# Kernel tuning notes

Measured on AMD Instinct MI355X. Metric: run time of the kernel, lower is better.

Reference implementation:

```python
import jax, jax.numpy as jnp
import numpy as np

D_MODEL, D_K, D_V, N_HEADS, D_FF = 1024, 64, 64, 16, 2736
EPS_NORM = 1e-12   # F.normalize eps
EPS_RMS = 1e-6     # RMSNorm eps


def _rmsnorm(x, g):
    return x * jax.lax.rsqrt(jnp.mean(x * x, axis=-1, keepdims=True) + EPS_RMS) * g


def _l2norm(x):
    n = jnp.sqrt(jnp.sum(x * x, axis=-1, keepdims=True))
    return x / jnp.maximum(n, EPS_NORM)


def setup_inputs() -> dict:
    key = jax.random.key(0)
    ks = jax.random.split(key, 10)
    B, T = 2, 1024
    s_in = 0.1 / np.sqrt(D_MODEL)   # xavier-like small init, gain 0.1
    s_ff = 0.1 / np.sqrt(D_FF)
    return {
        "x": jax.random.normal(ks[0], (B, T, D_MODEL), jnp.float32),
        "Wq": jax.random.normal(ks[1], (D_MODEL, N_HEADS * D_K), jnp.float32) * s_in,
        "Wk": jax.random.normal(ks[2], (D_MODEL, N_HEADS * D_K), jnp.float32) * s_in,
        "Wv": jax.random.normal(ks[3], (D_MODEL, N_HEADS * D_V), jnp.float32) * s_in,
        "Wg": jax.random.normal(ks[4], (D_MODEL, N_HEADS * D_K), jnp.float32) * s_in,
        "Wo": jax.random.normal(ks[5], (N_HEADS * D_V, D_MODEL), jnp.float32) * s_in,
        "w1": jax.random.normal(ks[6], (D_MODEL, D_FF), jnp.float32) * s_in,
        "w2": jax.random.normal(ks[7], (D_MODEL, D_FF), jnp.float32) * s_in,
        "w3": jax.random.normal(ks[8], (D_FF, D_MODEL), jnp.float32) * s_ff,
        "g_attn": jnp.ones((D_MODEL,), jnp.float32),
        "g_ffn": jnp.ones((D_MODEL,), jnp.float32),
    }


def _gla(h, Wq, Wk, Wv, Wg, Wo):
    B, T, _ = h.shape
    q = _l2norm((h @ Wq).reshape(B, T, N_HEADS, D_K))
    k = _l2norm((h @ Wk).reshape(B, T, N_HEADS, D_K))
    v = (h @ Wv).reshape(B, T, N_HEADS, D_V)
    alpha = jax.nn.sigmoid(h @ Wg).reshape(B, T, N_HEADS, D_K)

    def step(S, inp):
        a_t, k_t, v_t, q_t = inp                       # [B,H,dk],[B,H,dk],[B,H,dv],[B,H,dk]
        S = a_t[..., None] * S + k_t[..., None] * v_t[..., None, :]   # [B,H,dk,dv]
        o_t = jnp.einsum('bhkv,bhk->bhv', S, q_t)
        return S, o_t

    S0 = jnp.zeros((B, N_HEADS, D_K, D_V), h.dtype)
    xs = (jnp.swapaxes(alpha, 0, 1), jnp.swapaxes(k, 0, 1),
          jnp.swapaxes(v, 0, 1), jnp.swapaxes(q, 0, 1))  # time-major [T,B,H,*]
    _, o = jax.lax.scan(step, S0, xs)                    # o: [T,B,H,dv]
    o = jnp.swapaxes(o, 0, 1).reshape(B, T, N_HEADS * D_V)
    return o @ Wo


def reference(x, Wq, Wk, Wv, Wg, Wo, w1, w2, w3, g_attn, g_ffn):
    # Pre-LN GLA block: x -> Norm -> GLA -> +res -> Norm -> SwiGLU -> +res
    h = _rmsnorm(x, g_attn)
    x = x + _gla(h, Wq, Wk, Wv, Wg, Wo)
    h = _rmsnorm(x, g_ffn)
    ffn = (jax.nn.silu(h @ w1) * (h @ w2)) @ w3
    return x + ffn
```

## Files before the change

kernel.cpp:

```cpp
#include <hip/hip_runtime.h>

typedef unsigned short ushort_t;
typedef unsigned int uint32;
typedef short short8 __attribute__((ext_vector_type(8)));
typedef unsigned short ushort4v __attribute__((ext_vector_type(4)));
typedef float f32x4 __attribute__((ext_vector_type(4)));

#define MROWS 2048
#define DMODEL 1024
#define NH 16
#define DFF 2736
#define DFFP 2752
#define NBH 32

__device__ __forceinline__ float b2f(ushort_t u) {
  return __builtin_bit_cast(float, ((uint32)u) << 16);
}
__device__ __forceinline__ ushort_t f2b(float f) {
  uint32 u = __builtin_bit_cast(uint32, f);
  return (ushort_t)((u + 0x7FFFu + ((u >> 16) & 1u)) >> 16);
}
__device__ __forceinline__ float san(float v) {
  uint32 u = __builtin_bit_cast(uint32, v);
  return (((u >> 23) & 0xFFu) == 0xFFu) ? 0.0f : v;
}
__device__ __forceinline__ float sclamp(float v, float lim) {
  return fminf(fmaxf(san(v), -lim), lim);
}

typedef const __attribute__((address_space(1))) unsigned int* gas_ptr;
typedef __attribute__((address_space(3))) unsigned int* las_ptr;
__device__ __forceinline__ void gl_lds16(const void* g, void* l) {
  __builtin_amdgcn_global_load_lds((gas_ptr)g, (las_ptr)l, 16, 0, 0);
}

__device__ __forceinline__ void rmsnorm_body(
    const float* __restrict__ x, const float* __restrict__ g,
    ushort_t* __restrict__ out, int row, int tid) {
  size_t base = (size_t)row * DMODEL;
  int c0 = tid * 4;
  float4 t = *(const float4*)(x + base + c0);
  float v[4] = {t.x, t.y, t.z, t.w};
  float s = v[0]*v[0] + v[1]*v[1] + v[2]*v[2] + v[3]*v[3];
  for (int off = 32; off > 0; off >>= 1) s += __shfl_xor(s, off);
  __shared__ float red[4];
  int wave = tid >> 6, lane = tid & 63;
  if (lane == 0) red[wave] = s;
  __syncthreads();
  if (tid == 0) {
    float tt = red[0] + red[1] + red[2] + red[3];
    red[0] = rsqrtf(tt * (1.0f / DMODEL) + 1e-6f);
  }
  __syncthreads();
  float sc = red[0];
  float4 gg = *(const float4*)(g + c0);
  float gv[4] = {gg.x, gg.y, gg.z, gg.w};
  for (int j = 0; j < 4; ++j)
    out[base + c0 + j] = f2b(sclamp(v[j] * sc * gv[j], 1e4f));
}

__global__ __launch_bounds__(256) void rmsnorm_kernel(
    const float* __restrict__ x, const float* __restrict__ g,
    ushort_t* __restrict__ out) {
  rmsnorm_body(x, g, out, blockIdx.x, threadIdx.x);
}

__device__ __forceinline__ void transpose_tile(
    const float* __restrict__ src, ushort_t* __restrict__ d,
    int K, int N, int Kpad, int n0, int k0, int tid) {
  __shared__ ushort_t tile[32][33];
  int tx = tid & 31, ty = tid >> 5;
  #pragma unroll
  for (int i = 0; i < 4; ++i) {
    int k = k0 + ty + i * 8, n = n0 + tx;
    float v = (k < K && n < N) ? src[(size_t)k * N + n] : 0.0f;
    tile[ty + i * 8][tx] = f2b(v);
  }
  __syncthreads();
  #pragma unroll
  for (int i = 0; i < 4; ++i) {
    int r = ty + i * 8;
    d[(size_t)(n0 + r) * Kpad + k0 + tx] = tile[tx][r];
  }
}

__global__ __launch_bounds__(256) void transpose_kernel(
    const float* __restrict__ S0, const float* __restrict__ S1,
    const float* __restrict__ S2, const float* __restrict__ S3,
    ushort_t* __restrict__ dst, int K, int N, int Kpad, int Npad) {
  const float* src = (blockIdx.z == 0) ? S0 : (blockIdx.z == 1) ? S1
                   : (blockIdx.z == 2) ? S2 : S3;
  ushort_t* d = dst + (size_t)blockIdx.z * Npad * Kpad;
  transpose_tile(src, d, K, N, Kpad, blockIdx.x * 32, blockIdx.y * 32,
                 threadIdx.x);
}

__global__ __launch_bounds__(256) void transpose5_kernel(
    const float* __restrict__ S0, const float* __restrict__ S1,
    const float* __restrict__ S2, const float* __restrict__ S3,
    const float* __restrict__ S4,
    ushort_t* __restrict__ dA, ushort_t* __restrict__ dB) {
  int z = blockIdx.z;
  const float* src = (z == 0) ? S0 : (z == 1) ? S1 : (z == 2) ? S2
                   : (z == 3) ? S3 : S4;
  ushort_t* d = (z < 4) ? (dA + (size_t)z * 1024 * 1024) : dB;
  transpose_tile(src, d, 1024, 1024, 1024, blockIdx.x * 32, blockIdx.y * 32,
                 threadIdx.x);
}

__global__ __launch_bounds__(256) void setup_kernel(
    const float* __restrict__ x, const float* __restrict__ gat,
    ushort_t* __restrict__ h1,
    const float* __restrict__ Wq, const float* __restrict__ Wk,
    const float* __restrict__ Wv, const float* __restrict__ Wg,
    const float* __restrict__ Wo,
    ushort_t* __restrict__ dQKVG, ushort_t* __restrict__ dWo,
    const float* __restrict__ w1, const float* __restrict__ w2,
    const float* __restrict__ w3,
    ushort_t* __restrict__ dW12, ushort_t* __restrict__ dW3) {
  int bid = blockIdx.x, tid = threadIdx.x;
  if (bid < 2048) {
    rmsnorm_body(x, gat, h1, bid, tid);
  } else if (bid < 7168) {
    int idx = bid - 2048;
    int z = idx >> 10, rem = idx & 1023;
    const float* src = (z == 0) ? Wq : (z == 1) ? Wk : (z == 2) ? Wv
                     : (z == 3) ? Wg : Wo;
    ushort_t* d = (z < 4) ? (dQKVG + (size_t)z * 1024 * 1024) : dWo;
    transpose_tile(src, d, 1024, 1024, 1024, (rem & 31) * 32, (rem >> 5) * 32,
                   tid);
  } else {
    int fidx = bid - 7168;
    const float* src; ushort_t* d; int K, N, Kpad, bx, by;
    if (fidx < 5504) {
      int z = fidx / 2752, t = fidx % 2752;
      src = z ? w2 : w1; d = dW12 + (size_t)z * DFFP * 1024;
      K = 1024; N = DFF; Kpad = 1024;
      bx = t % 86; by = t / 86;
    } else {
      int t2 = fidx - 5504;
      src = w3; d = dW3;
      K = DFF; N = 1024; Kpad = DFFP;
      bx = t2 % 32; by = t2 / 32;
    }
    transpose_tile(src, d, K, N, Kpad, bx * 32, by * 32, tid);
  }
}

template<int MODE, int BM, int BN, int NB, int MINB>
__global__ __launch_bounds__(256, MINB) void gemm_kernel(
    const ushort_t* __restrict__ A, int lda,
    const ushort_t* __restrict__ Bt, int ldb, size_t boff, int K,
    float* __restrict__ outf, ushort_t* __restrict__ outb, int ldc,
    const float* __restrict__ resf) {
  constexpr int WM = BM / 2, WN = BN / 2;
  constexpr int MF = WM / 16, FN = WN / 16;
  __shared__ __align__(16) ushort_t As0[BM * 64];
  __shared__ __align__(16) ushort_t As1[BM * 64];
  __shared__ __align__(16) ushort_t Bs0[NB][BN * 64];
  __shared__ __align__(16) ushort_t Bs1[NB][BN * 64];
  int tid = threadIdx.x;
  int wave = tid >> 6, lane = tid & 63;
  int nwg = gridDim.x * gridDim.y;
  int orig = blockIdx.y * gridDim.x + blockIdx.x;
  int swz = (orig & 7) * (nwg >> 3) + (orig >> 3);
  int n0 = (swz / gridDim.y) * BN, m0 = (swz % gridDim.y) * BM;
  int wm = (wave >> 1) * WM, wn = (wave & 1) * WN;
  int arow = lane >> 3;
  int scol = (((lane & 7) ^ arow) & 7) * 8;
  int fm = lane & 15, fk = (lane >> 4) * 8;
  int xsw = (fm & 7) * 8;
  f32x4 zero = {0.f, 0.f, 0.f, 0.f};
  f32x4 acc[MF][FN];
  f32x4 acc2[NB == 2 ? MF : 1][NB == 2 ? FN : 1];
  #pragma unroll
  for (int i = 0; i < MF; ++i)
    #pragma unroll
    for (int j = 0; j < FN; ++j) {
      acc[i][j] = zero;
      if (NB == 2) acc2[i][j] = zero;
    }
  int nK = K >> 6;
  auto stage = [&](ushort_t (&Ad)[BM * 64], ushort_t (&Bd)[NB][BN * 64],
                   int kt) {
    int k0 = kt << 6;
    #pragma unroll
    for (int i = 0; i < BM / 32; ++i) {
      int g = i * 4 + wave;
      gl_lds16(A + (size_t)(m0 + g * 8 + arow) * lda + k0 + scol, &Ad[g * 512]);
    }
    #pragma unroll
    for (int nb = 0; nb < NB; ++nb)
      #pragma unroll
      for (int i = 0; i < BN / 32; ++i) {
        int g = i * 4 + wave;
        gl_lds16(Bt + nb * boff + (size_t)(n0 + g * 8 + arow) * ldb + k0 + scol,
                 &Bd[nb][g * 512]);
      }
  };
  auto compute = [&](const ushort_t (&Ad)[BM * 64],
                     const ushort_t (&Bd)[NB][BN * 64]) {
    #pragma unroll
    for (int kk = 0; kk < 64; kk += 32) {
      short8 a[MF];
      #pragma unroll
      for (int fi = 0; fi < MF; ++fi)
        a[fi] = *(const short8*)
            &Ad[(wm + fi * 16 + fm) * 64 + ((kk + fk) ^ xsw)];
      #pragma unroll
      for (int fj = 0; fj < FN; ++fj) {
        short8 b = *(const short8*)
            &Bd[0][(wn + fj * 16 + fm) * 64 + ((kk + fk) ^ xsw)];
        #pragma unroll
        for (int fi = 0; fi < MF; ++fi)
          acc[fi][fj] =
              __builtin_amdgcn_mfma_f32_16x16x32_bf16(a[fi], b, acc[fi][fj], 0, 0, 0);
        if (NB == 2) {
          short8 b2 = *(const short8*)
              &Bd[1][(wn + fj * 16 + fm) * 64 + ((kk + fk) ^ xsw)];
          #pragma unroll
          for (int fi = 0; fi < MF; ++fi)
            acc2[fi][fj] =
                __builtin_amdgcn_mfma_f32_16x16x32_bf16(a[fi], b2, acc2[fi][fj], 0, 0, 0);
        }
      }
    }
  };
  stage(As0, Bs0, 0);
  __syncthreads();
  int t = 0;
  for (;;) {
    if (t + 1 < nK) stage(As1, Bs1, t + 1);
    compute(As0, Bs0);
    __syncthreads();
    if (++t == nK) break;
    if (t + 1 < nK) stage(As0, Bs0, t + 1);
    compute(As1, Bs1);
    __syncthreads();
    if (++t == nK) break;
  }
  int rbase = m0 + wm + ((lane >> 4) << 2);
  #pragma unroll
  for (int fi = 0; fi < MF; ++fi)
    #pragma unroll
    for (int fj = 0; fj < FN; ++fj) {
      int col = n0 + wn + fj * 16 + fm;
      #pragma unroll
      for (int reg = 0; reg < 4; ++reg) {
        int row = rbase + fi * 16 + reg;
        float v = acc[fi][fj][reg];
        size_t oidx = (size_t)row * ldc + col;
        if (MODE == 0) {
          outb[oidx] = f2b(sclamp(v, 1e4f));
        } else if (MODE == 1) {
          outf[oidx] = sclamp(v, 0.25f) + resf[oidx];
        } else if (MODE == 2) {
          float y2 = sclamp(acc2[fi][fj][reg], 1e4f);
          float vc = fminf(fmaxf(san(v), -30.f), 30.f);
          float sg = vc / (1.0f + __expf(-vc));
          outb[oidx] = f2b(sclamp(sg * y2, 1e4f));
        } else {
          outf[oidx] = sclamp(v, 0.6f) + resf[oidx];
        }
      }
    }
}

template<int MODE, int BM, int BN, int MINB>
__global__ __launch_bounds__(256, MINB) void gemm_p3_kernel(
    const ushort_t* __restrict__ A, int lda,
    const ushort_t* __restrict__ Bt, int ldb, int K,
    float* __restrict__ outf, int ldc, const float* __restrict__ resf) {
  constexpr int WM = BM / 2, WN = BN / 2;
  constexpr int MF = WM / 16, FN = WN / 16;
  constexpr int L = BM / 32 + BN / 32;
  __shared__ __align__(16) ushort_t A0[BM * 64];
  __shared__ __align__(16) ushort_t A1[BM * 64];
  __shared__ __align__(16) ushort_t A2[BM * 64];
  __shared__ __align__(16) ushort_t B0[BN * 64];
  __shared__ __align__(16) ushort_t B1[BN * 64];
  __shared__ __align__(16) ushort_t B2[BN * 64];
  int tid = threadIdx.x;
  int wave = tid >> 6, lane = tid & 63;
  int nwg = gridDim.x * gridDim.y;
  int orig = blockIdx.y * gridDim.x + blockIdx.x;
  int swz = (orig & 7) * (nwg >> 3) + (orig >> 3);
  int n0 = (swz / gridDim.y) * BN, m0 = (swz % gridDim.y) * BM;
  int wm = (wave >> 1) * WM, wn = (wave & 1) * WN;
  int arow = lane >> 3;
  int scol = (((lane & 7) ^ arow) & 7) * 8;
  int fm = lane & 15, fk = (lane >> 4) * 8;
  int xsw = (fm & 7) * 8;
  f32x4 zero = {0.f, 0.f, 0.f, 0.f};
  f32x4 acc[MF][FN];
  #pragma unroll
  for (int i = 0; i < MF; ++i)
    #pragma unroll
    for (int j = 0; j < FN; ++j) acc[i][j] = zero;
  int nK = K >> 6;
  auto stage = [&](ushort_t (&Ad)[BM * 64], ushort_t (&Bd)[BN * 64], int kt) {
    int k0 = kt << 6;
    #pragma unroll
    for (int i = 0; i < BM / 32; ++i) {
      int g = i * 4 + wave;
      gl_lds16(A + (size_t)(m0 + g * 8 + arow) * lda + k0 + scol, &Ad[g * 512]);
    }
    #pragma unroll
    for (int i = 0; i < BN / 32; ++i) {
      int g = i * 4 + wave;
      gl_lds16(Bt + (size_t)(n0 + g * 8 + arow) * ldb + k0 + scol, &Bd[g * 512]);
    }
  };
  auto compute = [&](const ushort_t (&Ad)[BM * 64],
                     const ushort_t (&Bd)[BN * 64]) {
    #pragma unroll
    for (int kk = 0; kk < 64; kk += 32) {
      short8 a[MF];
      #pragma unroll
      for (int fi = 0; fi < MF; ++fi)
        a[fi] = *(const short8*)
            &Ad[(wm + fi * 16 + fm) * 64 + ((kk + fk) ^ xsw)];
      #pragma unroll
      for (int fj = 0; fj < FN; ++fj) {
        short8 b = *(const short8*)
            &Bd[(wn + fj * 16 + fm) * 64 + ((kk + fk) ^ xsw)];
        #pragma unroll
        for (int fi = 0; fi < MF; ++fi)
          acc[fi][fj] =
              __builtin_amdgcn_mfma_f32_16x16x32_bf16(a[fi], b, acc[fi][fj], 0, 0, 0);
      }
    }
  };
  auto wait_cnt = [&](int t) {
    if (t + 1 < nK) asm volatile("s_waitcnt vmcnt(%0)" :: "n"(L) : "memory");
    else            asm volatile("s_waitcnt vmcnt(0)" ::: "memory");
  };
  stage(A0, B0, 0);
  if (nK > 1) stage(A1, B1, 1);
  int t = 0;
  for (;;) {
    wait_cnt(t);
    __builtin_amdgcn_s_barrier();
    if (t + 2 < nK) stage(A2, B2, t + 2);
    compute(A0, B0);
    if (++t == nK) break;
    wait_cnt(t);
    __builtin_amdgcn_s_barrier();
    if (t + 2 < nK) stage(A0, B0, t + 2);
    compute(A1, B1);
    if (++t == nK) break;
    wait_cnt(t);
    __builtin_amdgcn_s_barrier();
    if (t + 2 < nK) stage(A1, B1, t + 2);
    compute(A2, B2);
    if (++t == nK) break;
  }
  int rbase = m0 + wm + ((lane >> 4) << 2);
  #pragma unroll
  for (int fi = 0; fi < MF; ++fi)
    #pragma unroll
    for (int fj = 0; fj < FN; ++fj) {
      int col = n0 + wn + fj * 16 + fm;
      #pragma unroll
      for (int reg = 0; reg < 4; ++reg) {
        int row = rbase + fi * 16 + reg;
        float v = acc[fi][fj][reg];
        size_t oidx = (size_t)row * ldc + col;
        if (MODE == 1) outf[oidx] = sclamp(v, 0.25f) + resf[oidx];
        else           outf[oidx] = sclamp(v, 0.6f) + resf[oidx];
      }
    }
}

template<int MODE>
__global__ __launch_bounds__(256) void gemm64_kernel(
    const ushort_t* __restrict__ A, int lda,
    const float* __restrict__ Bq, const float* __restrict__ Bk,
    const float* __restrict__ Bv, const float* __restrict__ Bg,
    int ldb, int K, int Nb,
    float* __restrict__ outf, ushort_t* __restrict__ outb, int ldc,
    const float* __restrict__ resf) {
  constexpr int NB = (MODE == 2) ? 2 : 1;
  __shared__ __align__(16) ushort_t As[64][72];
  __shared__ __align__(16) ushort_t Bs[NB][64][72];
  int tid = threadIdx.x;
  int wave = tid >> 6, lane = tid & 63;
  int m0 = blockIdx.y * 64;
  int n0 = blockIdx.x * 64;
  const float* B = Bq;
  int bcol = n0;
  f32x4 zero = {0.f, 0.f, 0.f, 0.f};
  f32x4 acc[4];
  f32x4 acc2[NB == 2 ? 4 : 1];
  for (int i = 0; i < 4; ++i) acc[i] = zero;
  if (NB == 2) for (int i = 0; i < 4; ++i) acc2[i] = zero;
  int r  = tid >> 2;
  int cb = (tid & 3) << 4;
  int fm = lane & 15;
  int fk = (lane >> 4) << 3;
  int nK = (K + 63) >> 6;
  for (int kt = 0; kt < nK; ++kt) {
    int k0 = kt << 6;
    for (int cc = 0; cc < 16; cc += 8) {
      int c = cb + cc;
      short8 val = {0,0,0,0,0,0,0,0};
      if (k0 + c + 8 <= K)
        val = *(const short8*)(A + (size_t)(m0 + r) * lda + k0 + c);
      *(short8*)&As[r][c] = val;
    }
    for (int nb = 0; nb < NB; ++nb) {
      const float* Bp = (nb == 0) ? B : Bk;
      for (int cc = 0; cc < 16; cc += 8) {
        int c = cb + cc;
        ushort_t val[8] = {0,0,0,0,0,0,0,0};
        if (k0 + r < K && bcol + c + 8 <= Nb) {
          const float* src = Bp + (size_t)(k0 + r) * ldb + bcol + c;
          float4 f0 = *(const float4*)(src);
          float4 f1 = *(const float4*)(src + 4);
          val[0] = f2b(f0.x); val[1] = f2b(f0.y);
          val[2] = f2b(f0.z); val[3] = f2b(f0.w);
          val[4] = f2b(f1.x); val[5] = f2b(f1.y);
          val[6] = f2b(f1.z); val[7] = f2b(f1.w);
        }
        for (int j = 0; j < 8; ++j) Bs[nb][c + j][r] = val[j];
      }
    }
    __syncthreads();
    for (int kk = 0; kk < 64; kk += 32) {
      short8 a = *(const short8*)&As[wave * 16 + fm][kk + fk];
      for (int nt = 0; nt < 4; ++nt) {
        short8 b = *(const short8*)&Bs[0][nt * 16 + fm][kk + fk];
        acc[nt] = __builtin_amdgcn_mfma_f32_16x16x32_bf16(a, b, acc[nt], 0, 0, 0);
        if (NB == 2) {
          short8 b2 = *(const short8*)&Bs[1][nt * 16 + fm][kk + fk];
          acc2[nt] = __builtin_amdgcn_mfma_f32_16x16x32_bf16(a, b2, acc2[nt], 0, 0, 0);
        }
      }
    }
    __syncthreads();
  }
  int rbase = m0 + wave * 16 + ((lane >> 4) << 2);
  for (int nt = 0; nt < 4; ++nt) {
    int col = n0 + nt * 16 + (lane & 15);
    for (int reg = 0; reg < 4; ++reg) {
      int row = rbase + reg;
      float v = acc[nt][reg];
      size_t oidx = (size_t)row * ldc + col;
      if (MODE == 2) {
        if (col < Nb) {
          float y2 = sclamp(acc2[nt][reg], 1e4f);
          float vc = fminf(fmaxf(san(v), -30.f), 30.f);
          float sg = vc / (1.0f + __expf(-vc));
          outb[oidx] = f2b(sclamp(sg * y2, 1e4f));
        }
      } else if (MODE == 3) {
        outf[oidx] = sclamp(v, 0.6f) + resf[oidx];
      }
    }
  }
}

__global__ __launch_bounds__(256) void prep_kernel(ushort_t* __restrict__ yq,
                                                   float* __restrict__ Bc) {
  int h = blockIdx.x, g = blockIdx.y;
  int bh = (g >> 4) * NH + h;
  int c = g & 15;
  int r0 = g * 64;
  int tid = threadIdx.x, wave = tid >> 6, lane = tid & 63;
  __shared__ float qs[64][65], ks[64][65], gs[64][65];
  for (int t = wave; t < 64; t += 4) {
    size_t rb = (size_t)(r0 + t) * 4096 + h * 64 + lane;
    float q = san(b2f(yq[rb]));
    float s = q * q;
    for (int off = 32; off > 0; off >>= 1) s += __shfl_xor(s, off);
    qs[t][lane] = q / fmaxf(sqrtf(s), 1e-12f);
    float k = san(b2f(yq[rb + 1024]));
    s = k * k;
    for (int off = 32; off > 0; off >>= 1) s += __shfl_xor(s, off);
    ks[t][lane] = k / fmaxf(sqrtf(s), 1e-12f);
    float a = fminf(fmaxf(san(b2f(yq[rb + 3072])), -30.f), 30.f);
    gs[t][lane] = 1.0f / (1.0f + __expf(-a));
  }
  __syncthreads();
  for (int j = 0; j < 16; ++j) {
    int kd = wave * 16 + j;
    float b = gs[lane][kd];
    #pragma unroll
    for (int off = 1; off < 64; off <<= 1) {
      float p = __shfl_up(b, off);
      if (lane >= off) b *= p;
    }
    b = fmaxf(b, 1e-28f);
    float inv = fminf(1.0f / b, 1e26f);
    qs[lane][kd] = sclamp(qs[lane][kd] * b, 1e30f);
    ks[lane][kd] = sclamp(ks[lane][kd] * inv, 1e30f);
    if (lane == 63) Bc[((size_t)bh * 16 + c) * 64 + kd] = b;
  }
  __syncthreads();
  for (int t = wave; t < 64; t += 4) {
    size_t rb = (size_t)(r0 + t) * 4096 + h * 64 + lane;
    yq[rb] = f2b(qs[t][lane]);
    yq[rb + 1024] = f2b(ks[t][lane]);
  }
}

__global__ __launch_bounds__(256) void prep_ktv_kernel(
    ushort_t* __restrict__ yq, float* __restrict__ Bc,
    float* __restrict__ KtV) {
  int h = blockIdx.x, g = blockIdx.y;
  int bh = (g >> 4) * NH + h;
  int c = g & 15;
  int r0 = g * 64;
  int tid = threadIdx.x, wave = tid >> 6, lane = tid & 63;
  __shared__ float qs[64][65], ks[64][65], gs[64][65];
  __shared__ ushort_t Kt[64][72];
  __shared__ ushort_t Vt[64][72];
  for (int t = wave; t < 64; t += 4) {
    size_t rb = (size_t)(r0 + t) * 4096 + h * 64 + lane;
    float q = san(b2f(yq[rb]));
    float s = q * q;
    for (int off = 32; off > 0; off >>= 1) s += __shfl_xor(s, off);
    qs[t][lane] = q / fmaxf(sqrtf(s), 1e-12f);
    float k = san(b2f(yq[rb + 1024]));
    s = k * k;
    for (int off = 32; off > 0; off >>= 1) s += __shfl_xor(s, off);
    ks[t][lane] = k / fmaxf(sqrtf(s), 1e-12f);
    float a = fminf(fmaxf(san(b2f(yq[rb + 3072])), -30.f), 30.f);
    gs[t][lane] = 1.0f / (1.0f + __expf(-a));
  }
  for (int i = tid; i < 512; i += 256) {
    int t = i >> 3, v8 = (i & 7) * 8;
    short8 v8v = *(const short8*)(yq + (size_t)(r0 + t) * 4096 + 2048 +
                                  h * 64 + v8);
    #pragma unroll
    for (int j = 0; j < 8; ++j) Vt[v8 + j][t] = (ushort_t)v8v[j];
  }
  __syncthreads();
  for (int j = 0; j < 16; ++j) {
    int kd = wave * 16 + j;
    float b = gs[lane][kd];
    #pragma unroll
    for (int off = 1; off < 64; off <<= 1) {
      float p = __shfl_up(b, off);
      if (lane >= off) b *= p;
    }
    b = fmaxf(b, 1e-28f);
    float inv = fminf(1.0f / b, 1e26f);
    qs[lane][kd] = sclamp(qs[lane][kd] * b, 1e30f);
    ks[lane][kd] = sclamp(ks[lane][kd] * inv, 1e30f);
    if (lane == 63) Bc[((size_t)bh * 16 + c) * 64 + kd] = b;
  }
  __syncthreads();
  for (int t = wave; t < 64; t += 4) {
    size_t rb = (size_t)(r0 + t) * 4096 + h * 64 + lane;
    yq[rb] = f2b(qs[t][lane]);
    ushort_t kb = f2b(ks[t][lane]);
    yq[rb + 1024] = kb;
    Kt[lane][t] = kb;
  }
  __syncthreads();
  int wm = wave * 16;
  int fm = lane & 15, fk = (lane >> 4) * 8;
  f32x4 zero = {0.f, 0.f, 0.f, 0.f};
  f32x4 acc[4] = {zero, zero, zero, zero};
  #pragma unroll
  for (int kk = 0; kk < 64; kk += 32) {
    short8 a = *(const short8*)&Kt[wm + fm][kk + fk];
    #pragma unroll
    for (int f = 0; f < 4; ++f) {
      short8 b = *(const short8*)&Vt[f * 16 + fm][kk + fk];
      acc[f] = __builtin_amdgcn_mfma_f32_16x16x32_bf16(a, b, acc[f], 0, 0, 0);
    }
  }
  size_t obase = (((size_t)bh * 16 + c) * 64) * 64;
  int krow = wm + ((lane >> 4) << 2);
  #pragma unroll
  for (int f = 0; f < 4; ++f) {
    int v = f * 16 + fm;
    #pragma unroll
    for (int reg = 0; reg < 4; ++reg)
      KtV[obase + (size_t)(krow + reg) * 64 + v] = acc[f][reg];
  }
}

__global__ __launch_bounds__(256) void scan_kernel(
    const float* __restrict__ KtV, const float* __restrict__ Bc,
    ushort_t* __restrict__ Sbuf) {
  int q = blockIdx.x, bh = blockIdx.y;
  int tid = threadIdx.x;
  int v4 = tid & 15, kloc = tid >> 4;
  int k = q * 16 + kloc;
  float4 S = {0.f, 0.f, 0.f, 0.f};
  size_t base = ((size_t)bh * 16) * 4096 + (size_t)k * 64 + v4 * 4;
  #pragma unroll
  for (int c = 0; c < 16; ++c) {
    size_t a = base + (size_t)c * 4096;
    ushort4v sb = {f2b(sclamp(S.x, 1e6f)), f2b(sclamp(S.y, 1e6f)),
                   f2b(sclamp(S.z, 1e6f)), f2b(sclamp(S.w, 1e6f))};
    *(ushort4v*)(Sbuf + a) = sb;
    float4 kv = *(const float4*)(KtV + a);
    float bc = Bc[((size_t)bh * 16 + c) * 64 + k];
    S.x = sclamp((S.x + kv.x) * bc, 1e6f);
    S.y = sclamp((S.y + kv.y) * bc, 1e6f);
    S.z = sclamp((S.z + kv.z) * bc, 1e6f);
    S.w = sclamp((S.w + kv.w) * bc, 1e6f);
  }
}

__global__ __launch_bounds__(256) void state_kernel(
    const ushort_t* __restrict__ yq, const float* __restrict__ Bc,
    ushort_t* __restrict__ Sbuf) {
  int vs = blockIdx.x;
  int bh = blockIdx.y;
  int bidx = bh >> 4, h = bh & 15;
  int tid = threadIdx.x;
  int k = tid & 63, v4 = tid >> 6;
  __shared__ float kbs[64][64];
  __shared__ float vls[64][16];
  float S[4] = {0.f, 0.f, 0.f, 0.f};
  for (int c = 0; c < 16; ++c) {
    size_t sb = (((size_t)bh * 16 + c) * 64 + k) * 64 + vs * 16 + v4 * 4;
    ushort4v st = {f2b(sclamp(S[0], 1e6f)), f2b(sclamp(S[1], 1e6f)),
                   f2b(sclamp(S[2], 1e6f)), f2b(sclamp(S[3], 1e6f))};
    *(ushort4v*)(Sbuf + sb) = st;
    int r0 = bidx * 1024 + c * 64;
    for (int i = tid; i < 4096; i += 256) {
      int t = i >> 6, kk = i & 63;
      kbs[t][kk] = b2f(yq[(size_t)(r0 + t) * 4096 + 1024 + h * 64 + kk]);
    }
    for (int i = tid; i < 1024; i += 256) {
      int t = i >> 4, vv = i & 15;
      vls[t][vv] = b2f(yq[(size_t)(r0 + t) * 4096 + 2048 + h * 64 + vs * 16 + vv]);
    }
    __syncthreads();
    for (int t = 0; t < 64; ++t) {
      float kv = kbs[t][k];
      S[0] += kv * vls[t][v4 * 4 + 0];
      S[1] += kv * vls[t][v4 * 4 + 1];
      S[2] += kv * vls[t][v4 * 4 + 2];
      S[3] += kv * vls[t][v4 * 4 + 3];
    }
    float bc = Bc[((size_t)bh * 16 + c) * 64 + k];
    S[0] = sclamp(S[0] * bc, 1e6f); S[1] = sclamp(S[1] * bc, 1e6f);
    S[2] = sclamp(S[2] * bc, 1e6f); S[3] = sclamp(S[3] * bc, 1e6f);
    __syncthreads();
  }
}

__global__ __launch_bounds__(256) void outk_kernel(
    const ushort_t* __restrict__ yq, const ushort_t* __restrict__ Sbuf,
    ushort_t* __restrict__ o) {
  int h = blockIdx.x;
  int g = blockIdx.y;
  int bh = (g >> 4) * NH + h;
  int c = g & 15;
  int r0 = g * 64;
  int tid = threadIdx.x, wave = tid >> 6, lane = tid & 63;
  __shared__ ushort_t Qs[64][72];
  __shared__ ushort_t Kbs[64][72];
  __shared__ ushort_t Vt[64][72];
  __shared__ ushort_t St[64][72];
  __shared__ ushort_t Ps[64][72];
  for (int i = tid; i < 512; i += 256) {
    int t = i >> 3, k8 = (i & 7) * 8;
    size_t rb = (size_t)(r0 + t) * 4096 + h * 64 + k8;
    *(short8*)&Qs[t][k8]  = *(const short8*)(yq + rb);
    *(short8*)&Kbs[t][k8] = *(const short8*)(yq + rb + 1024);
    short8 v8 = *(const short8*)(yq + rb + 2048);
    #pragma unroll
    for (int j = 0; j < 8; ++j) Vt[k8 + j][t] = (ushort_t)v8[j];
  }
  size_t sbase = (((size_t)bh * 16 + c) * 64) * 64;
  for (int i = tid; i < 1024; i += 256) {
    int kd = i >> 4, v4 = (i & 15) * 4;
    ushort4v s4 = *(const ushort4v*)(Sbuf + sbase + (size_t)kd * 64 + v4);
    St[v4 + 0][kd] = s4.x;
    St[v4 + 1][kd] = s4.y;
    St[v4 + 2][kd] = s4.z;
    St[v4 + 3][kd] = s4.w;
  }
  __syncthreads();
  int wm = wave * 16;
  int fm = lane & 15, fk = (lane >> 4) * 8;
  f32x4 zero = {0.f, 0.f, 0.f, 0.f};
  f32x4 oacc[4] = {zero, zero, zero, zero};
  f32x4 pacc[4] = {zero, zero, zero, zero};
  #pragma unroll
  for (int kk = 0; kk < 64; kk += 32) {
    short8 a = *(const short8*)&Qs[wm + fm][kk + fk];
    #pragma unroll
    for (int f = 0; f < 4; ++f) {
      short8 bS = *(const short8*)&St[f * 16 + fm][kk + fk];
      oacc[f] = __builtin_amdgcn_mfma_f32_16x16x32_bf16(a, bS, oacc[f], 0, 0, 0);
      short8 bK = *(const short8*)&Kbs[f * 16 + fm][kk + fk];
      pacc[f] = __builtin_amdgcn_mfma_f32_16x16x32_bf16(a, bK, pacc[f], 0, 0, 0);
    }
  }
  int prow = wm + ((lane >> 4) << 2);
  #pragma unroll
  for (int f = 0; f < 4; ++f) {
    int s = f * 16 + fm;
    #pragma unroll
    for (int reg = 0; reg < 4; ++reg) {
      float pv = (s <= prow + reg) ? pacc[f][reg] : 0.0f;
      Ps[prow + reg][s] = f2b(pv);
    }
  }
  __syncthreads();
  #pragma unroll
  for (int kk = 0; kk < 64; kk += 32) {
    short8 a = *(const short8*)&Ps[wm + fm][kk + fk];
    #pragma unroll
    for (int f = 0; f < 4; ++f) {
      short8 bV = *(const short8*)&Vt[f * 16 + fm][kk + fk];
      oacc[f] = __builtin_amdgcn_mfma_f32_16x16x32_bf16(a, bV, oacc[f], 0, 0, 0);
    }
  }
  #pragma unroll
  for (int f = 0; f < 4; ++f) {
    int v = f * 16 + fm;
    #pragma unroll
    for (int reg = 0; reg < 4; ++reg) {
      int row = prow + reg;
      o[(size_t)(r0 + row) * 1024 + h * 64 + v] = f2b(sclamp(oacc[f][reg], 100.f));
    }
  }
}

__global__ void sentinel_kernel(float* __restrict__ out, int env) {
  if (threadIdx.x == 0 && blockIdx.x == 0)
    out[0] = 1.0e6f + 1000.0f * (float)env;
}

extern "C" void kernel_launch(void* const* d_in, const int* in_sizes, int n_in,
                              void* d_out, int out_size, void* d_ws, size_t ws_size,
                              hipStream_t stream) {
  const float* x    = (const float*)d_in[0];
  const float* Wq   = (const float*)d_in[1];
  const float* Wk   = (const float*)d_in[2];
  const float* Wv   = (const float*)d_in[3];
  const float* Wg   = (const float*)d_in[4];
  const float* Wo   = (const float*)d_in[5];
  const float* w1   = (const float*)d_in[6];
  const float* w2   = (const float*)d_in[7];
  const float* w3   = (const float*)d_in[8];
  const float* gat  = (const float*)d_in[9];
  const float* gff  = (const float*)d_in[10];
  float* out = (float*)d_out;

  char* ws = (char*)d_ws;
  const size_t R0o = 0;
  const size_t R1o = (size_t)16 * 1024 * 1024;
  const size_t R2o = (size_t)20 * 1024 * 1024;
  const size_t R3o = R2o + 128 * 1024;
  const size_t R4o = R3o + (size_t)8 * 1024 * 1024;
  const size_t W12B = (size_t)2 * DFFP * 1024 * 2;
  const size_t W3B  = (size_t)1024 * DFFP * 2;
  const size_t R5o  = R4o + (size_t)16 * 1024 * 1024;
  const size_t NEED_SMALL = R4o + 4096;
  const size_t NEED_BIG   = R4o + W12B + 4096;
  const size_t NEED_BIG2  = R5o + W12B + W3B + 4096;

  ushort_t* yq     = (ushort_t*)(ws + R0o);
  ushort_t* ff     = (ushort_t*)(ws + R0o);
  ushort_t* h1     = (ushort_t*)(ws + R1o);
  ushort_t* obuf   = (ushort_t*)(ws + R1o);
  ushort_t* h2     = (ushort_t*)(ws + R1o);
  float*    Bc     = (float*)   (ws + R2o);
  ushort_t* BtQKVG = (ushort_t*)(ws + R3o);
  ushort_t* Sbuf   = (ushort_t*)(ws + R3o);
  float*    x2     = (float*)   (ws + R3o);
  float*    KtV    = (float*)   (ws + R4o);

  int env = 0;
  if (ws_size < NEED_SMALL) env |= 1;
  if (n_in != 11) env |= 2;
  if (in_sizes[0] != 2097152) env |= 4;
  if (n_in == 11 && (in_sizes[1] != 1048576 || in_sizes[6] != 1024 * 2736 ||
                     in_sizes[8] != 2736 * 1024 || in_sizes[9] != 1024)) env |= 8;
  if (out_size != 2097152) env |= 16;
  if (env) {
    sentinel_kernel<<<1, 64, 0, stream>>>(out, env);
    return;
  }
  bool big  = (ws_size >= NEED_BIG);
  bool big2 = (ws_size >= NEED_BIG2);
  ushort_t* BtWo = big ? (ushort_t*)(ws + R4o + (size_t)8 * 1024 * 1024)
                       : (ushort_t*)(ws + R0o);
  ushort_t* BtW12 = (ushort_t*)(ws + R5o);
  ushort_t* BtW3  = (ushort_t*)(ws + R5o + W12B);

  if (big2) {
    setup_kernel<<<15424, 256, 0, stream>>>(
        x, gat, h1, Wq, Wk, Wv, Wg, Wo, BtQKVG, BtWo, w1, w2, w3, BtW12, BtW3);
  } else {
    rmsnorm_kernel<<<MROWS, 256, 0, stream>>>(x, gat, h1);
    if (big) {
      transpose5_kernel<<<dim3(32, 32, 5), 256, 0, stream>>>(
          Wq, Wk, Wv, Wg, Wo, BtQKVG, BtWo);
    } else {
      transpose_kernel<<<dim3(32, 32, 4), 256, 0, stream>>>(
          Wq, Wk, Wv, Wg, BtQKVG, 1024, 1024, 1024, 1024);
    }
  }
  gemm_kernel<0, 128, 128, 1, 2><<<dim3(32, 16), 256, 0, stream>>>(
      h1, DMODEL, BtQKVG, DMODEL, 0, DMODEL, nullptr, yq, 4096, nullptr);
  if (big) {
    prep_ktv_kernel<<<dim3(16, 32), 256, 0, stream>>>(yq, Bc, KtV);
    scan_kernel<<<dim3(4, 32), 256, 0, stream>>>(KtV, Bc, Sbuf);
  } else {
    prep_kernel<<<dim3(16, 32), 256, 0, stream>>>(yq, Bc);
    state_kernel<<<dim3(4, 32), 256, 0, stream>>>(yq, Bc, Sbuf);
  }
  outk_kernel<<<dim3(16, 32), 256, 0, stream>>>(yq, Sbuf, obuf);
  if (!big)
    transpose_kernel<<<dim3(32, 32, 1), 256, 0, stream>>>(
        Wo, nullptr, nullptr, nullptr, BtWo, 1024, 1024, 1024, 1024);
  gemm_p3_kernel<1, 32, 64, 4><<<dim3(16, 64), 256, 0, stream>>>(
      obuf, DMODEL, BtWo, DMODEL, DMODEL, x2, DMODEL, x);
  rmsnorm_kernel<<<MROWS, 256, 0, stream>>>(x2, gff, h2);
  if (big2) {
    gemm_kernel<2, 128, 64, 2, 2><<<dim3(43, 16), 256, 0, stream>>>(
        h2, DMODEL, BtW12, DMODEL, (size_t)DFFP * 1024, DMODEL,
        nullptr, ff, DFFP, nullptr);
    gemm_p3_kernel<3, 32, 64, 4><<<dim3(16, 64), 256, 0, stream>>>(
        ff, DFFP, BtW3, DFFP, DFFP, out, DMODEL, x2);
  } else {
    gemm64_kernel<2><<<dim3(43, 32), 256, 0, stream>>>(
        h2, DMODEL, w1, w2, nullptr, nullptr, DFF, DMODEL, DFF,
        nullptr, ff, DFF, nullptr);
    gemm64_kernel<3><<<dim3(16, 32), 256, 0, stream>>>(
        ff, DFF, w3, nullptr, nullptr, nullptr, DMODEL, DFF, DMODEL,
        out, nullptr, DMODEL, x2);
  }
}
```

Measured before the change: 257.2 us.

## Merge chunked GLA prep, scan and output kernels into one cooperative kernel

The chunked GLA stages (intra-chunk KtV prep, inter-chunk state scan, chunk output) are moved into device functions and run from a single cooperative kernel, with grid-wide syncs between stages. The aim is to remove two kernel launch gaps and the drain/refill between dependent kernels. Risks: grid.sync costs, 512 blocks with 68KB of shared memory each must all be co-resident or the cooperative launch fails and falls back, and only 128 blocks do work during the scan phase.

```diff
diff --git a/kernel.cpp b/kernel.cpp
--- a/kernel.cpp
+++ b/kernel.cpp
@@ -1,4 +1,5 @@
 #include <hip/hip_runtime.h>
+#include <hip/hip_cooperative_groups.h>
 
 typedef unsigned short ushort_t;
 typedef unsigned int uint32;
@@ -504,17 +505,18 @@
   }
 }
 
-__global__ __launch_bounds__(256) void prep_ktv_kernel(
+__device__ __forceinline__ void prep_ktv_body(
     ushort_t* __restrict__ yq, float* __restrict__ Bc,
-    float* __restrict__ KtV) {
-  int h = blockIdx.x, g = blockIdx.y;
+    float* __restrict__ KtV, char* smem, int h, int g, int tid) {
   int bh = (g >> 4) * NH + h;
   int c = g & 15;
   int r0 = g * 64;
-  int tid = threadIdx.x, wave = tid >> 6, lane = tid & 63;
-  __shared__ float qs[64][65], ks[64][65], gs[64][65];
-  __shared__ ushort_t Kt[64][72];
-  __shared__ ushort_t Vt[64][72];
+  int wave = tid >> 6, lane = tid & 63;
+  float (*qs)[65] = (float(*)[65])(smem);
+  float (*ks)[65] = (float(*)[65])(smem + 16640);
+  float (*gs)[65] = (float(*)[65])(smem + 33280);
+  ushort_t (*Kt)[72] = (ushort_t(*)[72])(smem + 49920);
+  ushort_t (*Vt)[72] = (ushort_t(*)[72])(smem + 59136);
   for (int t = wave; t < 64; t += 4) {
     size_t rb = (size_t)(r0 + t) * 4096 + h * 64 + lane;
     float q = san(b2f(yq[rb]));
@@ -583,11 +585,9 @@
   }
 }
 
-__global__ __launch_bounds__(256) void scan_kernel(
+__device__ __forceinline__ void scan_body(
     const float* __restrict__ KtV, const float* __restrict__ Bc,
-    ushort_t* __restrict__ Sbuf) {
-  int q = blockIdx.x, bh = blockIdx.y;
-  int tid = threadIdx.x;
+    ushort_t* __restrict__ Sbuf, int q, int bh, int tid) {
   int v4 = tid & 15, kloc = tid >> 4;
   int k = q * 16 + kloc;
   float4 S = {0.f, 0.f, 0.f, 0.f};
@@ -605,6 +605,117 @@
     S.z = sclamp((S.z + kv.z) * bc, 1e6f);
     S.w = sclamp((S.w + kv.w) * bc, 1e6f);
   }
+}
+
+__device__ __forceinline__ void outk_body(
+    const ushort_t* __restrict__ yq, const ushort_t* __restrict__ Sbuf,
+    ushort_t* __restrict__ o, char* smem, int h, int g, int tid) {
+  int bh = (g >> 4) * NH + h;
+  int c = g & 15;
+  int r0 = g * 64;
+  int wave = tid >> 6, lane = tid & 63;
+  ushort_t (*Qs)[72]  = (ushort_t(*)[72])(smem);
+  ushort_t (*Kbs)[72] = (ushort_t(*)[72])(smem + 9216);
+  ushort_t (*Vt)[72]  = (ushort_t(*)[72])(smem + 18432);
+  ushort_t (*St)[72]  = (ushort_t(*)[72])(smem + 27648);
+  ushort_t (*Ps)[72]  = (ushort_t(*)[72])(smem + 36864);
+  for (int i = tid; i < 512; i += 256) {
+    int t = i >> 3, k8 = (i & 7) * 8;
+    size_t rb = (size_t)(r0 + t) * 4096 + h * 64 + k8;
+    *(short8*)&Qs[t][k8]  = *(const short8*)(yq + rb);
+    *(short8*)&Kbs[t][k8] = *(const short8*)(yq + rb + 1024);
+    short8 v8 = *(const short8*)(yq + rb + 2048);
+    #pragma unroll
+    for (int j = 0; j < 8; ++j) Vt[k8 + j][t] = (ushort_t)v8[j];
+  }
+  size_t sbase = (((size_t)bh * 16 + c) * 64) * 64;
+  for (int i = tid; i < 1024; i += 256) {
+    int kd = i >> 4, v4 = (i & 15) * 4;
+    ushort4v s4 = *(const ushort4v*)(Sbuf + sbase + (size_t)kd * 64 + v4);
+    St[v4 + 0][kd] = s4.x;
+    St[v4 + 1][kd] = s4.y;
+    St[v4 + 2][kd] = s4.z;
+    St[v4 + 3][kd] = s4.w;
+  }
+  __syncthreads();
+  int wm = wave * 16;
+  int fm = lane & 15, fk = (lane >> 4) * 8;
+  f32x4 zero = {0.f, 0.f, 0.f, 0.f};
+  f32x4 oacc[4] = {zero, zero, zero, zero};
+  f32x4 pacc[4] = {zero, zero, zero, zero};
+  #pragma unroll
+  for (int kk = 0; kk < 64; kk += 32) {
+    short8 a = *(const short8*)&Qs[wm + fm][kk + fk];
+    #pragma unroll
+    for (int f = 0; f < 4; ++f) {
+      short8 bS = *(const short8*)&St[f * 16 + fm][kk + fk];
+      oacc[f] = __builtin_amdgcn_mfma_f32_16x16x32_bf16(a, bS, oacc[f], 0, 0, 0);
+      short8 bK = *(const short8*)&Kbs[f * 16 + fm][kk + fk];
+      pacc[f] = __builtin_amdgcn_mfma_f32_16x16x32_bf16(a, bK, pacc[f], 0, 0, 0);
+    }
+  }
+  int prow = wm + ((lane >> 4) << 2);
+  #pragma unroll
+  for (int f = 0; f < 4; ++f) {
+    int s = f * 16 + fm;
+    #pragma unroll
+    for (int reg = 0; reg < 4; ++reg) {
+      float pv = (s <= prow + reg) ? pacc[f][reg] : 0.0f;
+      Ps[prow + reg][s] = f2b(pv);
+    }
+  }
+  __syncthreads();
+  #pragma unroll
+  for (int kk = 0; kk < 64; kk += 32) {
+    short8 a = *(const short8*)&Ps[wm + fm][kk + fk];
+    #pragma unroll
+    for (int f = 0; f < 4; ++f) {
+      short8 bV = *(const short8*)&Vt[f * 16 + fm][kk + fk];
+      oacc[f] = __builtin_amdgcn_mfma_f32_16x16x32_bf16(a, bV, oacc[f], 0, 0, 0);
+    }
+  }
+  #pragma unroll
+  for (int f = 0; f < 4; ++f) {
+    int v = f * 16 + fm;
+    #pragma unroll
+    for (int reg = 0; reg < 4; ++reg) {
+      int row = prow + reg;
+      o[(size_t)(r0 + row) * 1024 + h * 64 + v] = f2b(sclamp(oacc[f][reg], 100.f));
+    }
+  }
+}
+
+__global__ __launch_bounds__(256) void prep_ktv_kernel(
+    ushort_t* __restrict__ yq, float* __restrict__ Bc,
+    float* __restrict__ KtV) {
+  __shared__ __align__(16) char smem[68352];
+  prep_ktv_body(yq, Bc, KtV, smem, blockIdx.x, blockIdx.y, threadIdx.x);
+}
+
+__global__ __launch_bounds__(256) void scan_kernel(
+    const float* __restrict__ KtV, const float* __restrict__ Bc,
+    ushort_t* __restrict__ Sbuf) {
+  scan_body(KtV, Bc, Sbuf, blockIdx.x, blockIdx.y, threadIdx.x);
+}
+
+__global__ __launch_bounds__(256) void outk_kernel(
+    const ushort_t* __restrict__ yq, const ushort_t* __restrict__ Sbuf,
+    ushort_t* __restrict__ o) {
+  __shared__ __align__(16) char smem[46080];
+  outk_body(yq, Sbuf, o, smem, blockIdx.x, blockIdx.y, threadIdx.x);
+}
+
+__global__ __launch_bounds__(256) void mid_kernel(
+    ushort_t* yq, float* Bc, float* KtV, ushort_t* Sbuf, ushort_t* o) {
+  namespace cg = cooperative_groups;
+  cg::grid_group grid = cg::this_grid();
+  __shared__ __align__(16) char smem[68352];
+  int bx = blockIdx.x, by = blockIdx.y, tid = threadIdx.x;
+  prep_ktv_body(yq, Bc, KtV, smem, bx, by, tid);
+  grid.sync();
+  if (bx < 4) scan_body(KtV, Bc, Sbuf, bx, by, tid);
+  grid.sync();
+  outk_body(yq, Sbuf, o, smem, bx, by, tid);
 }
 
 __global__ __launch_bounds__(256) void state_kernel(
@@ -647,86 +758,6 @@
   }
 }
 
-__global__ __launch_bounds__(256) void outk_kernel(
-    const ushort_t* __restrict__ yq, const ushort_t* __restrict__ Sbuf,
-    ushort_t* __restrict__ o) {
-  int h = blockIdx.x;
-  int g = blockIdx.y;
-  int bh = (g >> 4) * NH + h;
-  int c = g & 15;
-  int r0 = g * 64;
-  int tid = threadIdx.x, wave = tid >> 6, lane = tid & 63;
-  __shared__ ushort_t Qs[64][72];
-  __shared__ ushort_t Kbs[64][72];
-  __shared__ ushort_t Vt[64][72];
-  __shared__ ushort_t St[64][72];
-  __shared__ ushort_t Ps[64][72];
-  for (int i = tid; i < 512; i += 256) {
-    int t = i >> 3, k8 = (i & 7) * 8;
-    size_t rb = (size_t)(r0 + t) * 4096 + h * 64 + k8;
-    *(short8*)&Qs[t][k8]  = *(const short8*)(yq + rb);
-    *(short8*)&Kbs[t][k8] = *(const short8*)(yq + rb + 1024);
-    short8 v8 = *(const short8*)(yq + rb + 2048);
-    #pragma unroll
-    for (int j = 0; j < 8; ++j) Vt[k8 + j][t] = (ushort_t)v8[j];
-  }
-  size_t sbase = (((size_t)bh * 16 + c) * 64) * 64;
-  for (int i = tid; i < 1024; i += 256) {
-    int kd = i >> 4, v4 = (i & 15) * 4;
-    ushort4v s4 = *(const ushort4v*)(Sbuf + sbase + (size_t)kd * 64 + v4);
-    St[v4 + 0][kd] = s4.x;
-    St[v4 + 1][kd] = s4.y;
-    St[v4 + 2][kd] = s4.z;
-    St[v4 + 3][kd] = s4.w;
-  }
-  __syncthreads();
-  int wm = wave * 16;
-  int fm = lane & 15, fk = (lane >> 4) * 8;
-  f32x4 zero = {0.f, 0.f, 0.f, 0.f};
-  f32x4 oacc[4] = {zero, zero, zero, zero};
-  f32x4 pacc[4] = {zero, zero, zero, zero};
-  #pragma unroll
-  for (int kk = 0; kk < 64; kk += 32) {
-    short8 a = *(const short8*)&Qs[wm + fm][kk + fk];
-    #pragma unroll
-    for (int f = 0; f < 4; ++f) {
-      short8 bS = *(const short8*)&St[f * 16 + fm][kk + fk];
-      oacc[f] = __builtin_amdgcn_mfma_f32_16x16x32_bf16(a, bS, oacc[f], 0, 0, 0);
-      short8 bK = *(const short8*)&Kbs[f * 16 + fm][kk + fk];
-      pacc[f] = __builtin_amdgcn_mfma_f32_16x16x32_bf16(a, bK, pacc[f], 0, 0, 0);
-    }
-  }
-  int prow = wm + ((lane >> 4) << 2);
-  #pragma unroll
-  for (int f = 0; f < 4; ++f) {
-    int s = f * 16 + fm;
-    #pragma unroll
-    for (int reg = 0; reg < 4; ++reg) {
-      float pv = (s <= prow + reg) ? pacc[f][reg] : 0.0f;
-      Ps[prow + reg][s] = f2b(pv);
-    }
-  }
-  __syncthreads();
-  #pragma unroll
-  for (int kk = 0; kk < 64; kk += 32) {
-    short8 a = *(const short8*)&Ps[wm + fm][kk + fk];
-    #pragma unroll
-    for (int f = 0; f < 4; ++f) {
-      short8 bV = *(const short8*)&Vt[f * 16 + fm][kk + fk];
-      oacc[f] = __builtin_amdgcn_mfma_f32_16x16x32_bf16(a, bV, oacc[f], 0, 0, 0);
-    }
-  }
-  #pragma unroll
-  for (int f = 0; f < 4; ++f) {
-    int v = f * 16 + fm;
-    #pragma unroll
-    for (int reg = 0; reg < 4; ++reg) {
-      int row = prow + reg;
-      o[(size_t)(r0 + row) * 1024 + h * 64 + v] = f2b(sclamp(oacc[f][reg], 100.f));
-    }
-  }
-}
-
 __global__ void sentinel_kernel(float* __restrict__ out, int env) {
   if (threadIdx.x == 0 && blockIdx.x == 0)
     out[0] = 1.0e6f + 1000.0f * (float)env;
@@ -806,13 +837,23 @@
   gemm_kernel<0, 128, 128, 1, 2><<<dim3(32, 16), 256, 0, stream>>>(
       h1, DMODEL, BtQKVG, DMODEL, 0, DMODEL, nullptr, yq, 4096, nullptr);
   if (big) {
-    prep_ktv_kernel<<<dim3(16, 32), 256, 0, stream>>>(yq, Bc, KtV);
-    scan_kernel<<<dim3(4, 32), 256, 0, stream>>>(KtV, Bc, Sbuf);
+    ushort_t* yq_a = yq; float* Bc_a = Bc; float* KtV_a = KtV;
+    ushort_t* Sb_a = Sbuf; ushort_t* o_a = obuf;
+    void* margs[] = {(void*)&yq_a, (void*)&Bc_a, (void*)&KtV_a,
+                     (void*)&Sb_a, (void*)&o_a};
+    hipError_t ce = hipLaunchCooperativeKernel(
+        (const void*)mid_kernel, dim3(16, 32), dim3(256), margs, 0, stream);
+    if (ce != hipSuccess) {
+      (void)hipGetLastError();
+      prep_ktv_kernel<<<dim3(16, 32), 256, 0, stream>>>(yq, Bc, KtV);
+      scan_kernel<<<dim3(4, 32), 256, 0, stream>>>(KtV, Bc, Sbuf);
+      outk_kernel<<<dim3(16, 32), 256, 0, stream>>>(yq, Sbuf, obuf);
+    }
   } else {
     prep_kernel<<<dim3(16, 32), 256, 0, stream>>>(yq, Bc);
     state_kernel<<<dim3(4, 32), 256, 0, stream>>>(yq, Bc, Sbuf);
-  }
-  outk_kernel<<<dim3(16, 32), 256, 0, stream>>>(yq, Sbuf, obuf);
+    outk_kernel<<<dim3(16, 32), 256, 0, stream>>>(yq, Sbuf, obuf);
+  }
   if (!big)
     transpose_kernel<<<dim3(32, 32, 1), 256, 0, stream>>>(
         Wo, nullptr, nullptr, nullptr, BtWo, 1024, 1024, 1024, 1024);
```

Measured after the change: 410.8 us. +59.7%, slower.
